# Optimization experiments

Hardware: AMD Instinct MI355X
Metric: run time of the kernel (lower is better)

## Reference

```python
import jax, jax.numpy as jnp
import numpy as np
from jax import lax

B, T, N, HID = 4, 144, 256, 64
CH, NC = 9, 4  # chunk_size_short, num_chunks_short


def setup_inputs():
    key = jax.random.key(0)
    ks = jax.random.split(key, 30)
    r = lambda i, sh, s=0.05: jax.random.normal(ks[i], sh, jnp.float32) * s
    adj = (jax.random.uniform(ks[1], (N, N)) < 0.1).astype(jnp.float32)
    adj = adj.at[jnp.arange(N), jnp.arange(N)].set(1.0)  # self-loops
    return {
        "seg": jax.random.normal(ks[0], (B, T, N, N), jnp.float32),
        "adj": adj,
        "dist": jax.random.uniform(ks[2], (N, N), jnp.float32),
        "W_gat": r(3, (N, HID)),
        "a_src": r(4, (HID,)),
        "a_dst": r(5, (HID,)),
        "lstm_Wih": r(6, (4 * HID, HID)),
        "lstm_Whh": r(7, (4 * HID, HID)),
        "lstm_bih": r(8, (4 * HID,)),
        "lstm_bhh": r(9, (4 * HID,)),
        "attnL_W": r(10, (HID, HID)),
        "attnL_b": r(11, (HID,)),
        "attnL_v": r(12, (HID,)),
        "gru_Wih": r(13, (NC, 3 * HID, HID)),
        "gru_Whh": r(14, (NC, 3 * HID, HID)),
        "gru_bih": r(15, (NC, 3 * HID)),
        "gru_bhh": r(16, (NC, 3 * HID)),
        "attnS_W": r(17, (NC, HID, HID)),
        "attnS_b": r(18, (NC, HID)),
        "attnS_v": r(19, (NC, HID)),
        "lin1_W": r(20, (2 * HID, HID + HID * NC)),
        "lin1_b": r(21, (2 * HID,)),
        "lin2_W": r(22, (N * N, 2 * HID)),
        "lin2_b": r(23, (N * N,)),
        "conv_k": r(24, (1, 1, 3, 3)),
        "conv_b": r(25, (1,)),
    }


def gat_features(seg, adj, dist, W_gat, a_src, a_dst):
    # Batches the per-timestep GAT over the time axis (B,T folded together).
    Wh = jnp.einsum('btnf,fh->btnh', seg, W_gat)                     # (B,T,N,H)
    e = jax.nn.leaky_relu((Wh @ a_src)[..., :, None] + (Wh @ a_dst)[..., None, :], 0.2)
    e = e - dist                                                     # distance penalty on logits
    logits = jnp.where(adj > 0, e, -1e9)                             # mask non-edges
    attn = jax.nn.softmax(logits, axis=-1)                           # (B,T,N,N)
    Hn = jax.nn.elu(jnp.einsum('btij,btjh->btih', attn, Wh))         # (B,T,N,H)
    return Hn.mean(axis=2)                                           # (B,T,H) mean-pool over nodes


def lstm(x, Wih, Whh, bih, bhh):
    h0 = jnp.zeros((x.shape[0], Whh.shape[1]), x.dtype)
    def step(carry, xt):
        h, c = carry
        g = xt @ Wih.T + bih + h @ Whh.T + bhh
        i, f, gg, o = jnp.split(g, 4, axis=-1)  # torch gate order i,f,g,o
        c = jax.nn.sigmoid(f) * c + jax.nn.sigmoid(i) * jnp.tanh(gg)
        h = jax.nn.sigmoid(o) * jnp.tanh(c)
        return (h, c), h
    _, ys = lax.scan(step, (h0, h0), jnp.swapaxes(x, 0, 1))
    return jnp.swapaxes(ys, 0, 1)


def gru(x, Wih, Whh, bih, bhh):
    h0 = jnp.zeros((x.shape[0], Whh.shape[1]), x.dtype)
    def step(h, xt):
        gx = xt @ Wih.T + bih
        gh = h @ Whh.T + bhh
        xr, xz, xn = jnp.split(gx, 3, axis=-1)  # torch gate order r,z,n
        hr, hz, hn = jnp.split(gh, 3, axis=-1)
        rr = jax.nn.sigmoid(xr + hr)
        zz = jax.nn.sigmoid(xz + hz)
        nn_ = jnp.tanh(xn + rr * hn)
        h = (1.0 - zz) * nn_ + zz * h
        return h, h
    _, ys = lax.scan(step, h0, jnp.swapaxes(x, 0, 1))
    return jnp.swapaxes(ys, 0, 1)


def tattn(h, W, b, v):
    s = jnp.tanh(h @ W + b) @ v          # (B,T) additive attention scores
    a = jax.nn.softmax(s, axis=1)
    return jnp.einsum('bt,bth->bh', a, h)


def reference(seg, adj, dist, W_gat, a_src, a_dst, lstm_Wih, lstm_Whh, lstm_bih, lstm_bhh,
              attnL_W, attnL_b, attnL_v, gru_Wih, gru_Whh, gru_bih, gru_bhh,
              attnS_W, attnS_b, attnS_v, lin1_W, lin1_b, lin2_W, lin2_b, conv_k, conv_b):
    Bsz = seg.shape[0]
    feats = gat_features(seg, adj, dist, W_gat, a_src, a_dst)        # (B,T,H)
    ctxL = tattn(lstm(feats, lstm_Wih, lstm_Whh, lstm_bih, lstm_bhh), attnL_W, attnL_b, attnL_v)
    # Short-term GCN features are the same GAT outputs on the last W_short steps.
    short = feats[:, -CH * NC:, :].reshape(Bsz, NC, CH, HID)
    gru_out = jax.vmap(gru, in_axes=(1, 0, 0, 0, 0), out_axes=1)(short, gru_Wih, gru_Whh, gru_bih, gru_bhh)
    ctxS = jax.vmap(tattn, in_axes=(1, 0, 0, 0), out_axes=1)(gru_out, attnS_W, attnS_b, attnS_v)  # (B,NC,H)
    fused = jnp.concatenate([ctxL, ctxS.reshape(Bsz, NC * HID)], axis=1)  # (B, 5H)
    h1 = jax.nn.relu(fused @ lin1_W.T + lin1_b)
    out = (h1 @ lin2_W.T + lin2_b).reshape(Bsz, 1, N, N)
    out = lax.conv_general_dilated(out, conv_k, (1, 1), 'SAME',
                                   dimension_numbers=('NCHW', 'OIHW', 'NCHW'))
    out = out + conv_b[None, :, None, None]
    return jax.nn.softplus(out[:, 0])
```

## Files before the change

kernel.cpp:

```cpp
#include <hip/hip_runtime.h>
#include <hip/hip_bf16.h>
#include <cstddef>


typedef __attribute__((ext_vector_type(8))) short bf16x8;
typedef __attribute__((ext_vector_type(4))) float f32x4;

__device__ __forceinline__ float sigf(float x) { return 1.0f / (1.0f + __expf(-x)); }
__device__ __forceinline__ float tanh_(float x) {
    x = fminf(fmaxf(x, -15.f), 15.f);
    float e = __expf(2.f * x);
    return (e - 1.f) / (e + 1.f);
}
__device__ __forceinline__ unsigned short f2b(float f) {
    unsigned u = __float_as_uint(f);
    u += 0x7FFFu + ((u >> 16) & 1u);
    return (unsigned short)(u >> 16);
}
__device__ __forceinline__ unsigned pk2(float lo, float hi) {
    __hip_bfloat162 h = __float22bfloat162_rn(float2{lo, hi});
    return *reinterpret_cast<unsigned*>(&h);
}
__device__ __forceinline__ float b2f(short s) {
    return __uint_as_float(((unsigned)(unsigned short)s) << 16);
}
__device__ __forceinline__ float rlane(float v, int k) {
    return __uint_as_float(__builtin_amdgcn_readlane(__float_as_uint(v), k));
}

__global__ void k_prep(const float* __restrict__ adj, const float* __restrict__ dist,
                       const float* __restrict__ W_gat,
                       unsigned short* __restrict__ Mb, unsigned short* __restrict__ Wt) {
    int blk = blockIdx.x, tid = threadIdx.x;
    if (blk < 256) {
        int i = blk * 256 + tid;
        Mb[i] = f2b((adj[i] > 0.f) ? -dist[i] : -1e9f);
    } else {
        for (int it = 0; it < 64; ++it) {
            int e = it * 256 + tid;
            int k = e >> 6, c = e & 63;
            Wt[c * 256 + k] = f2b(W_gat[e]);
        }
    }
}

__global__ __launch_bounds__(256, 6) void k_gatA(
    const float* __restrict__ seg, const unsigned short* __restrict__ Wt,
    const float* __restrict__ a_src, const float* __restrict__ a_dst,
    unsigned short* __restrict__ WhT, float* __restrict__ svec, float* __restrict__ dvec,
    float* __restrict__ smaxp, float* __restrict__ dmaxp) {
    __shared__ __align__(16) short A_s[64 * 64];
    __shared__ float red[8];

    const int tid  = threadIdx.x;
    const int lane = tid & 63;
    const int wv   = tid >> 6;
    const int blk  = blockIdx.x;
    const int bt   = blk >> 2;
    const int sub  = blk & 3;
    const float* __restrict__ segp = seg + (size_t)bt * 65536 + sub * 64 * 256;

    f32x4 acc[4];
    #pragma unroll
    for (int n = 0; n < 4; ++n) acc[n] = (f32x4)(0.f);

    for (int kc = 0; kc < 4; ++kc) {
        #pragma unroll
        for (int it = 0; it < 2; ++it) {
            int unit = it * 256 + tid;
            int row = unit >> 3, u = unit & 7;
            const float* g = segp + row * 256 + kc * 64 + u * 8;
            f32x4 v0 = *(const f32x4*)g;
            f32x4 v1 = *(const f32x4*)(g + 4);
            uint4 pk;
            pk.x = pk2(v0[0], v0[1]); pk.y = pk2(v0[2], v0[3]);
            pk.z = pk2(v1[0], v1[1]); pk.w = pk2(v1[2], v1[3]);
            *(uint4*)&A_s[(row * 8 + (u ^ (row & 7))) * 8] = pk;
        }
        bf16x8 bfr[2][4];
        #pragma unroll
        for (int kt2 = 0; kt2 < 2; ++kt2) {
            int ku = kt2 * 4 + (lane >> 4);
            #pragma unroll
            for (int nt = 0; nt < 4; ++nt) {
                int col = nt * 16 + (lane & 15);
                bfr[kt2][nt] = *(const bf16x8*)(Wt + col * 256 + kc * 64 + ku * 8);
            }
        }
        __syncthreads();
        int arow = wv * 16 + (lane & 15);
        #pragma unroll
        for (int kt2 = 0; kt2 < 2; ++kt2) {
            int ku = kt2 * 4 + (lane >> 4);
            bf16x8 afr = *(const bf16x8*)&A_s[(arow * 8 + (ku ^ (arow & 7))) * 8];
            #pragma unroll
            for (int nt = 0; nt < 4; ++nt)
                acc[nt] = __builtin_amdgcn_mfma_f32_16x16x32_bf16(afr, bfr[kt2][nt], acc[nt], 0, 0, 0);
        }
        __syncthreads();
    }

    float asv[4], adv[4];
    #pragma unroll
    for (int nt = 0; nt < 4; ++nt) {
        asv[nt] = a_src[nt * 16 + (lane & 15)];
        adv[nt] = a_dst[nt * 16 + (lane & 15)];
    }
    float mxs = -3e38f, mxd = -3e38f;
    int rowbase = sub * 64 + wv * 16;
    #pragma unroll
    for (int r = 0; r < 4; ++r) {
        float ps = acc[0][r] * asv[0] + acc[1][r] * asv[1] + acc[2][r] * asv[2] + acc[3][r] * asv[3];
        float pd = acc[0][r] * adv[0] + acc[1][r] * adv[1] + acc[2][r] * adv[2] + acc[3][r] * adv[3];
        #pragma unroll
        for (int m = 1; m < 16; m <<= 1) { ps += __shfl_xor(ps, m); pd += __shfl_xor(pd, m); }
        if ((lane & 15) == 0) {
            int row = rowbase + (lane >> 4) * 4 + r;
            svec[bt * 256 + row] = ps;
            dvec[bt * 256 + row] = pd;
        }
        mxs = fmaxf(mxs, ps); mxd = fmaxf(mxd, pd);
    }
    mxs = fmaxf(mxs, __shfl_xor(mxs, 16)); mxs = fmaxf(mxs, __shfl_xor(mxs, 32));
    mxd = fmaxf(mxd, __shfl_xor(mxd, 16)); mxd = fmaxf(mxd, __shfl_xor(mxd, 32));
    if (lane == 0) { red[wv] = mxs; red[4 + wv] = mxd; }

    {
        int c = lane & 15, q = lane >> 4;
        int kt2  = wv >> 1;
        int oct  = (wv & 1) * 2 + (q >> 1);
        int laneP = oct * 16 + c;
        int e0b  = (q & 1) * 8;
        #pragma unroll
        for (int nt = 0; nt < 4; ++nt) {
            uint2 pk4;
            pk4.x = pk2(acc[nt][0], acc[nt][1]);
            pk4.y = pk2(acc[nt][2], acc[nt][3]);
            *(uint2*)((char*)A_s + (((kt2 * 4 + nt) * 64 + laneP) * 16 + e0b)) = pk4;
        }
    }
    __syncthreads();
    {
        const uint4* Fs = (const uint4*)A_s;
        uint4* Gd = (uint4*)(WhT + (size_t)bt * 16384 + sub * 4096);
        Gd[tid] = Fs[tid];
        Gd[256 + tid] = Fs[256 + tid];
    }
    if (tid == 0) {
        smaxp[blk] = fmaxf(fmaxf(red[0], red[1]), fmaxf(red[2], red[3]));
        dmaxp[blk] = fmaxf(fmaxf(red[4], red[5]), fmaxf(red[6], red[7]));
    }
}

__global__ __launch_bounds__(256, 4) void k_gatBF(
    const unsigned short* __restrict__ WhT, const float* __restrict__ svec,
    const float* __restrict__ dvec, const float* __restrict__ smaxp,
    const float* __restrict__ dmaxp, const unsigned short* __restrict__ Mb,
    const float* __restrict__ lWih, const float* __restrict__ lbih,
    const float* __restrict__ lbhh, float* __restrict__ feats, float* __restrict__ gx) {
    __shared__ __align__(16) float dv_l[256];
    __shared__ float red[256];
    __shared__ __align__(16) float feats_l[64];

    const int tid  = threadIdx.x;
    const int lane = tid & 63;
    const int wv   = tid >> 6;
    const int wrow = wv * 64;
    const int bt   = blockIdx.x;
    const unsigned short* __restrict__ Wp = WhT + (size_t)bt * 16384;

    dv_l[tid] = dvec[bt * 256 + tid];
    float mB;
    {
        float ms = fmaxf(fmaxf(smaxp[bt * 4], smaxp[bt * 4 + 1]),
                         fmaxf(smaxp[bt * 4 + 2], smaxp[bt * 4 + 3]));
        float md = fmaxf(fmaxf(dmaxp[bt * 4], dmaxp[bt * 4 + 1]),
                         fmaxf(dmaxp[bt * 4 + 2], dmaxp[bt * 4 + 3]));
        float x = ms + md;
        mB = fmaxf(x, 0.2f * x);
    }
    float sv4[4];
    #pragma unroll
    for (int mt = 0; mt < 4; ++mt) sv4[mt] = svec[bt * 256 + wrow + mt * 16 + (lane & 15)];
    __syncthreads();

    f32x4 acc2[4][4];
    #pragma unroll
    for (int a = 0; a < 4; ++a)
        #pragma unroll
        for (int b = 0; b < 4; ++b) acc2[a][b] = (f32x4)(0.f);
    float psum[4] = {0.f, 0.f, 0.f, 0.f};
    const int jbase = (lane >> 4) * 8;

    #pragma unroll 1
    for (int kt = 0; kt < 8; ++kt) {
        int j0 = kt * 32 + jbase;
        bf16x8 bfr[4];
        #pragma unroll
        for (int nt = 0; nt < 4; ++nt)
            bfr[nt] = *(const bf16x8*)(Wp + ((kt * 4 + nt) * 64 + lane) * 8);
        f32x4 d0 = *(const f32x4*)&dv_l[j0];
        f32x4 d1 = *(const f32x4*)&dv_l[j0 + 4];
        #pragma unroll
        for (int mt = 0; mt < 4; ++mt) {
            int prow = wrow + mt * 16 + (lane & 15);
            bf16x8 mrow = *(const bf16x8*)(Mb + prow * 256 + j0);
            float p[8];
            #pragma unroll
            for (int e = 0; e < 4; ++e) {
                float u = sv4[mt] + d0[e];
                u = fmaxf(u, 0.2f * u);
                p[e] = __expf(u + b2f(mrow[e]) - mB);
                float w = sv4[mt] + d1[e];
                w = fmaxf(w, 0.2f * w);
                p[4 + e] = __expf(w + b2f(mrow[4 + e]) - mB);
            }
            psum[mt] += ((p[0] + p[1]) + (p[2] + p[3])) + ((p[4] + p[5]) + (p[6] + p[7]));
            uint4 upf;
            upf.x = pk2(p[0], p[1]); upf.y = pk2(p[2], p[3]);
            upf.z = pk2(p[4], p[5]); upf.w = pk2(p[6], p[7]);
            bf16x8 pf = *reinterpret_cast<bf16x8*>(&upf);
            #pragma unroll
            for (int nt = 0; nt < 4; ++nt)
                acc2[mt][nt] = __builtin_amdgcn_mfma_f32_16x16x32_bf16(pf, bfr[nt], acc2[mt][nt], 0, 0, 0);
        }
    }
    #pragma unroll
    for (int mt = 0; mt < 4; ++mt) {
        psum[mt] += __shfl_xor(psum[mt], 16);
        psum[mt] += __shfl_xor(psum[mt], 32);
    }

    float part[4] = {0.f, 0.f, 0.f, 0.f};
    #pragma unroll
    for (int mt = 0; mt < 4; ++mt) {
        #pragma unroll
        for (int r = 0; r < 4; ++r) {
            float rs  = __shfl(psum[mt], ((lane >> 4) << 2) + r);
            float inv = 1.0f / rs;
            #pragma unroll
            for (int nt = 0; nt < 4; ++nt) {
                float x = acc2[mt][nt][r] * inv;
                x = (x > 0.f) ? x : expm1f(x);
                part[nt] += x;
            }
        }
    }
    #pragma unroll
    for (int nt = 0; nt < 4; ++nt) {
        part[nt] += __shfl_xor(part[nt], 16);
        part[nt] += __shfl_xor(part[nt], 32);
    }
    if ((lane >> 4) == 0) {
        #pragma unroll
        for (int nt = 0; nt < 4; ++nt) red[wv * 64 + nt * 16 + lane] = part[nt];
    }
    __syncthreads();
    if (tid < 64) {
        float f = (red[tid] + red[64 + tid] + red[128 + tid] + red[192 + tid]) * (1.0f / 256.0f);
        feats[bt * 64 + tid] = f;
        feats_l[tid] = f;
    }
    __syncthreads();
    {
        float a = lbih[tid] + lbhh[tid];
        const float* wp = lWih + tid * 64;
        #pragma unroll
        for (int k4 = 0; k4 < 16; ++k4) {
            f32x4 w = *(const f32x4*)(wp + k4 * 4);
            f32x4 x = *(const f32x4*)&feats_l[k4 * 4];
            a += w[0] * x[0] + w[1] * x[1] + w[2] * x[2] + w[3] * x[3];
        }
        gx[bt * 256 + tid] = a;
    }
}

__global__ __launch_bounds__(256) void k_rnnctx(
    const float* __restrict__ gx, const float* __restrict__ lWhh,
    const float* __restrict__ aLW, const float* __restrict__ aLb, const float* __restrict__ aLv,
    const float* __restrict__ feats, const float* __restrict__ gWih,
    const float* __restrict__ gWhh, const float* __restrict__ gbih,
    const float* __restrict__ gbhh, const float* __restrict__ aSW,
    const float* __restrict__ aSb, const float* __restrict__ aSv,
    float* __restrict__ ctxL, float* __restrict__ ctxS) {
    __shared__ __align__(16) float smem[10048];
    int tid = threadIdx.x;
    if (blockIdx.x < 4) {
        int b = blockIdx.x;
        int lane = tid & 63, wv = tid >> 6;
        float* Hl = smem;
        float* gl = smem + 9216;
        float* sc = smem + 9728;
        float* al = smem + 9872;
        float wr[64];
        #pragma unroll
        for (int q = 0; q < 16; ++q)
            *(f32x4*)&wr[q * 4] = *(const f32x4*)&lWhh[tid * 64 + q * 4];
        float c_s = 0.f;
        float hprev = 0.f;
        float gx_cur = gx[(size_t)b * 36864 + tid];
        for (int t = 0; t < 144; ++t) {
            float gx_next = (t < 143) ? gx[((size_t)b * 144 + t + 1) * 256 + tid] : 0.f;
            float s0 = 0.f, s1 = 0.f, s2 = 0.f, s3 = 0.f;
            #pragma unroll
            for (int k = 0; k < 64; k += 4) {
                s0 += wr[k]     * rlane(hprev, k);
                s1 += wr[k + 1] * rlane(hprev, k + 1);
                s2 += wr[k + 2] * rlane(hprev, k + 2);
                s3 += wr[k + 3] * rlane(hprev, k + 3);
            }
            float a = gx_cur + ((s0 + s1) + (s2 + s3));
            gl[(t & 1) * 256 + tid] = a;
            __syncthreads();
            float ig = gl[(t & 1) * 256 + lane],       fg = gl[(t & 1) * 256 + 64 + lane],
                  gg = gl[(t & 1) * 256 + 128 + lane], og = gl[(t & 1) * 256 + 192 + lane];
            c_s = sigf(fg) * c_s + sigf(ig) * tanh_(gg);
            float h = sigf(og) * tanh_(c_s);
            hprev = h;
            if (wv == 0) Hl[t * 64 + lane] = h;
            gx_cur = gx_next;
        }
        __syncthreads();
        float wcol[64];
        #pragma unroll
        for (int k = 0; k < 64; ++k) wcol[k] = aLW[k * 64 + lane];
        float bb = aLb[lane], vv = aLv[lane];
        for (int g = 0; g < 36; ++g) {
            int t = g * 4 + wv;
            float acc = bb;
            #pragma unroll
            for (int q = 0; q < 16; ++q) {
                f32x4 h4 = *(const f32x4*)&Hl[t * 64 + q * 4];
                acc += wcol[q * 4 + 0] * h4[0] + wcol[q * 4 + 1] * h4[1]
                     + wcol[q * 4 + 2] * h4[2] + wcol[q * 4 + 3] * h4[3];
            }
            float p = tanh_(acc) * vv;
            #pragma unroll
            for (int m = 1; m < 64; m <<= 1) p += __shfl_xor(p, m);
            if (lane == 0) sc[t] = p;
        }
        __syncthreads();
        float mx = -3e38f;
        for (int t2 = 0; t2 < 144; ++t2) mx = fmaxf(mx, sc[t2]);
        float ss = 0.f;
        for (int t2 = 0; t2 < 144; ++t2) ss += __expf(sc[t2] - mx);
        float inv = 1.f / ss;
        if (tid < 144) al[tid] = __expf(sc[tid] - mx) * inv;
        __syncthreads();
        if (tid < 64) {
            float acc = 0.f;
            for (int t2 = 0; t2 < 144; ++t2) acc += al[t2] * Hl[t2 * 64 + tid];
            ctxL[b * 64 + tid] = acc;
        }
    } else {
        int bi_ = blockIdx.x - 4;
        int b = bi_ >> 2, c2 = bi_ & 3;
        float* hvg = smem;
        float* xvg = smem + 64;
        float* gxl = smem + 128;
        float* ghl = smem + 320;
        float* hst = smem + 512;
        float wi[64], wh[64], bi = 0.f, bh = 0.f, h_s = 0.f;
        if (tid < 192) {
            #pragma unroll
            for (int q = 0; q < 16; ++q) {
                *(f32x4*)&wi[q * 4] = *(const f32x4*)&gWih[(size_t)(c2 * 192 + tid) * 64 + q * 4];
                *(f32x4*)&wh[q * 4] = *(const f32x4*)&gWhh[(size_t)(c2 * 192 + tid) * 64 + q * 4];
            }
            bi = gbih[c2 * 192 + tid];
            bh = gbhh[c2 * 192 + tid];
        }
        if (tid < 64) hvg[tid] = 0.f;
        __syncthreads();
        for (int s = 0; s < 9; ++s) {
            int t = 108 + c2 * 9 + s;
            if (tid < 64) xvg[tid] = feats[(b * 144 + t) * 64 + tid];
            __syncthreads();
            if (tid < 192) {
                float ax = bi, ah = bh;
                float a0 = 0.f, a1 = 0.f, b0 = 0.f, b1 = 0.f;
                #pragma unroll
                for (int k = 0; k < 64; k += 2) {
                    a0 += wi[k] * xvg[k];     a1 += wi[k + 1] * xvg[k + 1];
                    b0 += wh[k] * hvg[k];     b1 += wh[k + 1] * hvg[k + 1];
                }
                gxl[tid] = ax + a0 + a1; ghl[tid] = ah + b0 + b1;
            }
            __syncthreads();
            if (tid < 64) {
                float xr = gxl[tid], xz = gxl[64 + tid], xn = gxl[128 + tid];
                float hr = ghl[tid], hz = ghl[64 + tid], hn = ghl[128 + tid];
                float rr = sigf(xr + hr), zz = sigf(xz + hz);
                float nn = tanh_(xn + rr * hn);
                h_s = (1.f - zz) * nn + zz * h_s;
                hvg[tid] = h_s;
                hst[s * 64 + tid] = h_s;
            }
            __syncthreads();
        }
        if (tid < 64) {
            int lane = tid;
            const float* Wc = aSW + c2 * 4096;
            float wcol[64];
            #pragma unroll
            for (int k = 0; k < 64; ++k) wcol[k] = Wc[k * 64 + lane];
            float bb = aSb[c2 * 64 + lane], vv = aSv[c2 * 64 + lane];
            float sv[9];
            #pragma unroll 1
            for (int s = 0; s < 9; ++s) {
                float acc = bb;
                #pragma unroll
                for (int q = 0; q < 16; ++q) {
                    f32x4 h4 = *(const f32x4*)&hst[s * 64 + q * 4];
                    acc += wcol[q * 4 + 0] * h4[0] + wcol[q * 4 + 1] * h4[1]
                         + wcol[q * 4 + 2] * h4[2] + wcol[q * 4 + 3] * h4[3];
                }
                float p = tanh_(acc) * vv;
                #pragma unroll
                for (int m = 1; m < 64; m <<= 1) p += __shfl_xor(p, m);
                sv[s] = p;
            }
            float mx = -3e38f;
            #pragma unroll
            for (int s = 0; s < 9; ++s) mx = fmaxf(mx, sv[s]);
            float ss = 0.f;
            #pragma unroll
            for (int s = 0; s < 9; ++s) { sv[s] = __expf(sv[s] - mx); ss += sv[s]; }
            float inv = 1.f / ss;
            float acc = 0.f;
            #pragma unroll
            for (int s = 0; s < 9; ++s) acc += sv[s] * inv * hst[s * 64 + lane];
            ctxS[(b * 4 + c2) * 64 + lane] = acc;
        }
    }
}

__global__ __launch_bounds__(512) void k_lin1(
    const float* __restrict__ ctxL, const float* __restrict__ ctxS,
    const float* __restrict__ W, const float* __restrict__ bb,
    float* __restrict__ h1) {
    int tid = threadIdx.x;
    __shared__ __align__(16) float fu[4 * 320];
    for (int c = tid; c < 1280; c += 512) {
        int b2 = c / 320, k = c % 320;
        fu[c] = (k < 64) ? ctxL[b2 * 64 + k] : ctxS[b2 * 256 + (k - 64)];
    }
    __syncthreads();
    int b = tid >> 7, r = tid & 127;
    float acc = bb[r];
    #pragma unroll 4
    for (int k4 = 0; k4 < 80; ++k4) {
        f32x4 w = *(const f32x4*)&W[r * 320 + k4 * 4];
        f32x4 x = *(const f32x4*)&fu[b * 320 + k4 * 4];
        acc += w[0] * x[0] + w[1] * x[1] + w[2] * x[2] + w[3] * x[3];
    }
    h1[b * 128 + r] = fmaxf(acc, 0.f);
}

__global__ __launch_bounds__(256) void k_lin2(
    const float* __restrict__ h1, const float* __restrict__ W,
    const float* __restrict__ bb, float* __restrict__ h2) {
    __shared__ __align__(16) float h1l[512];
    int tid = threadIdx.x, blk = blockIdx.x;
    for (int c = tid; c < 512; c += 256) h1l[c] = h1[c];
    __syncthreads();
    int r = blk * 64 + (tid >> 2);
    int q = tid & 3;
    const float* wp = W + (size_t)r * 128 + q * 32;
    float a0 = 0.f, a1 = 0.f, a2 = 0.f, a3 = 0.f;
    #pragma unroll
    for (int i = 0; i < 8; ++i) {
        f32x4 w  = *(const f32x4*)(wp + i * 4);
        f32x4 x0 = *(const f32x4*)&h1l[q * 32 + i * 4];
        f32x4 x1 = *(const f32x4*)&h1l[128 + q * 32 + i * 4];
        f32x4 x2 = *(const f32x4*)&h1l[256 + q * 32 + i * 4];
        f32x4 x3 = *(const f32x4*)&h1l[384 + q * 32 + i * 4];
        a0 += w[0] * x0[0] + w[1] * x0[1] + w[2] * x0[2] + w[3] * x0[3];
        a1 += w[0] * x1[0] + w[1] * x1[1] + w[2] * x1[2] + w[3] * x1[3];
        a2 += w[0] * x2[0] + w[1] * x2[1] + w[2] * x2[2] + w[3] * x2[3];
        a3 += w[0] * x3[0] + w[1] * x3[1] + w[2] * x3[2] + w[3] * x3[3];
    }
    a0 += __shfl_xor(a0, 1); a0 += __shfl_xor(a0, 2);
    a1 += __shfl_xor(a1, 1); a1 += __shfl_xor(a1, 2);
    a2 += __shfl_xor(a2, 1); a2 += __shfl_xor(a2, 2);
    a3 += __shfl_xor(a3, 1); a3 += __shfl_xor(a3, 2);
    if (q == 0) {
        float bv = bb[r];
        h2[r]             = a0 + bv;
        h2[65536 + r]     = a1 + bv;
        h2[2 * 65536 + r] = a2 + bv;
        h2[3 * 65536 + r] = a3 + bv;
    }
}

__global__ __launch_bounds__(256) void k_conv(
    const float* __restrict__ h2, const float* __restrict__ ck,
    const float* __restrict__ cb, float* __restrict__ out) {
    int x = threadIdx.x;
    int b = blockIdx.x >> 8, y = blockIdx.x & 255;
    float kk[9];
    #pragma unroll
    for (int i = 0; i < 9; ++i) kk[i] = ck[i];
    const float* base = h2 + b * 65536;
    float acc = cb[0];
    #pragma unroll
    for (int dy = -1; dy <= 1; ++dy) {
        int yy = y + dy;
        if (yy < 0 || yy > 255) continue;
        #pragma unroll
        for (int dx = -1; dx <= 1; ++dx) {
            int xx = x + dx;
            if (xx < 0 || xx > 255) continue;
            acc += base[yy * 256 + xx] * kk[(dy + 1) * 3 + (dx + 1)];
        }
    }
    float r = (acc > 20.f) ? acc : log1pf(__expf(acc));
    out[b * 65536 + y * 256 + x] = r;
}

extern "C" void kernel_launch(void* const* d_in, const int* in_sizes, int n_in,
                              void* d_out, int out_size, void* d_ws, size_t ws_size,
                              hipStream_t stream) {
    const float* seg   = (const float*)d_in[0];
    const float* adj   = (const float*)d_in[1];
    const float* dist  = (const float*)d_in[2];
    const float* W_gat = (const float*)d_in[3];
    const float* a_src = (const float*)d_in[4];
    const float* a_dst = (const float*)d_in[5];
    const float* lWih  = (const float*)d_in[6];
    const float* lWhh  = (const float*)d_in[7];
    const float* lbih  = (const float*)d_in[8];
    const float* lbhh  = (const float*)d_in[9];
    const float* aLW   = (const float*)d_in[10];
    const float* aLb   = (const float*)d_in[11];
    const float* aLv   = (const float*)d_in[12];
    const float* gWih  = (const float*)d_in[13];
    const float* gWhh  = (const float*)d_in[14];
    const float* gbih  = (const float*)d_in[15];
    const float* gbhh  = (const float*)d_in[16];
    const float* aSW   = (const float*)d_in[17];
    const float* aSb   = (const float*)d_in[18];
    const float* aSv   = (const float*)d_in[19];
    const float* l1W   = (const float*)d_in[20];
    const float* l1b   = (const float*)d_in[21];
    const float* l2W   = (const float*)d_in[22];
    const float* l2b   = (const float*)d_in[23];
    const float* ck    = (const float*)d_in[24];
    const float* cb    = (const float*)d_in[25];
    float* out = (float*)d_out;

    float* ws = (float*)d_ws;
    unsigned short* Mb  = (unsigned short*)ws;
    unsigned short* Wt  = (unsigned short*)(ws + 32768);
    float* svec  = ws + 40960;
    float* dvec  = svec + 147456;
    float* smaxp = dvec + 147456;
    float* dmaxp = smaxp + 2304;
    unsigned short* WhT = (unsigned short*)(dmaxp + 2304);
    float* feats = dmaxp + 2304 + 4718592;
    float* gx    = feats + 36864;
    float* ctxL  = gx + 147456;
    float* ctxS  = ctxL + 256;
    float* h1    = ctxS + 1024;
    float* h2    = h1 + 512;

    k_prep<<<257, 256, 0, stream>>>(adj, dist, W_gat, Mb, Wt);
    k_gatA<<<2304, 256, 0, stream>>>(seg, Wt, a_src, a_dst, WhT, svec, dvec, smaxp, dmaxp);
    k_gatBF<<<576, 256, 0, stream>>>(WhT, svec, dvec, smaxp, dmaxp, Mb, lWih, lbih, lbhh, feats, gx);
    k_rnnctx<<<20, 256, 0, stream>>>(gx, lWhh, aLW, aLb, aLv, feats, gWih, gWhh, gbih, gbhh,
                                     aSW, aSb, aSv, ctxL, ctxS);
    k_lin1<<<1, 512, 0, stream>>>(ctxL, ctxS, l1W, l1b, h1);
    k_lin2<<<1024, 256, 0, stream>>>(h1, l2W, l2b, h2);
    k_conv<<<1024, 256, 0, stream>>>(h2, ck, cb, out);
}
```

Baseline: 236.7 us.

## Run LSTM recurrence in a single wavefront to remove per-step block barriers

The LSTM recurrence now runs in one 64-lane wavefront. Each lane holds all four gate rows of Whh in registers (256 floats), so the per-timestep shared-memory exchange and __syncthreads are gone. The gate inputs are prefetched two steps ahead, and the sigmoid and tanh divides are replaced with hardware reciprocal approximations. The cost is four times more FMAs per lane on the serial path and heavy register pressure, hence launch_bounds(256,1), with a risk of spilling.

```diff
diff --git a/kernel.cpp b/kernel.cpp
--- a/kernel.cpp
+++ b/kernel.cpp
@@ -6,11 +6,12 @@
 typedef __attribute__((ext_vector_type(8))) short bf16x8;
 typedef __attribute__((ext_vector_type(4))) float f32x4;
 
-__device__ __forceinline__ float sigf(float x) { return 1.0f / (1.0f + __expf(-x)); }
+__device__ __forceinline__ float rcp_(float x) { return __builtin_amdgcn_rcpf(x); }
+__device__ __forceinline__ float sigf(float x) { return rcp_(1.0f + __expf(-x)); }
 __device__ __forceinline__ float tanh_(float x) {
     x = fminf(fmaxf(x, -15.f), 15.f);
     float e = __expf(2.f * x);
-    return (e - 1.f) / (e + 1.f);
+    return (e - 1.f) * rcp_(e + 1.f);
 }
 __device__ __forceinline__ unsigned short f2b(float f) {
     unsigned u = __float_as_uint(f);
@@ -275,7 +276,7 @@
     }
 }
 
-__global__ __launch_bounds__(256) void k_rnnctx(
+__global__ __launch_bounds__(256, 1) void k_rnnctx(
     const float* __restrict__ gx, const float* __restrict__ lWhh,
     const float* __restrict__ aLW, const float* __restrict__ aLb, const float* __restrict__ aLv,
     const float* __restrict__ feats, const float* __restrict__ gWih,
@@ -289,36 +290,49 @@
         int b = blockIdx.x;
         int lane = tid & 63, wv = tid >> 6;
         float* Hl = smem;
-        float* gl = smem + 9216;
-        float* sc = smem + 9728;
-        float* al = smem + 9872;
-        float wr[64];
-        #pragma unroll
-        for (int q = 0; q < 16; ++q)
-            *(f32x4*)&wr[q * 4] = *(const f32x4*)&lWhh[tid * 64 + q * 4];
-        float c_s = 0.f;
-        float hprev = 0.f;
-        float gx_cur = gx[(size_t)b * 36864 + tid];
-        for (int t = 0; t < 144; ++t) {
-            float gx_next = (t < 143) ? gx[((size_t)b * 144 + t + 1) * 256 + tid] : 0.f;
-            float s0 = 0.f, s1 = 0.f, s2 = 0.f, s3 = 0.f;
-            #pragma unroll
-            for (int k = 0; k < 64; k += 4) {
-                s0 += wr[k]     * rlane(hprev, k);
-                s1 += wr[k + 1] * rlane(hprev, k + 1);
-                s2 += wr[k + 2] * rlane(hprev, k + 2);
-                s3 += wr[k + 3] * rlane(hprev, k + 3);
-            }
-            float a = gx_cur + ((s0 + s1) + (s2 + s3));
-            gl[(t & 1) * 256 + tid] = a;
-            __syncthreads();
-            float ig = gl[(t & 1) * 256 + lane],       fg = gl[(t & 1) * 256 + 64 + lane],
-                  gg = gl[(t & 1) * 256 + 128 + lane], og = gl[(t & 1) * 256 + 192 + lane];
-            c_s = sigf(fg) * c_s + sigf(ig) * tanh_(gg);
-            float h = sigf(og) * tanh_(c_s);
-            hprev = h;
-            if (wv == 0) Hl[t * 64 + lane] = h;
-            gx_cur = gx_next;
+        float* sc = smem + 9216;
+        float* al = smem + 9360;
+        if (wv == 0) {
+            float wi_[64], wf_[64], wg_[64], wo_[64];
+            #pragma unroll
+            for (int q = 0; q < 16; ++q) {
+                *(f32x4*)&wi_[q * 4] = *(const f32x4*)&lWhh[(size_t)lane * 64 + q * 4];
+                *(f32x4*)&wf_[q * 4] = *(const f32x4*)&lWhh[(size_t)(64 + lane) * 64 + q * 4];
+                *(f32x4*)&wg_[q * 4] = *(const f32x4*)&lWhh[(size_t)(128 + lane) * 64 + q * 4];
+                *(f32x4*)&wo_[q * 4] = *(const f32x4*)&lWhh[(size_t)(192 + lane) * 64 + q * 4];
+            }
+            const float* gxb = gx + (size_t)b * 36864;
+            float c_s = 0.f, h = 0.f;
+            float gA0 = gxb[lane],       gA1 = gxb[64 + lane],
+                  gA2 = gxb[128 + lane], gA3 = gxb[192 + lane];
+            float gB0 = gxb[256 + lane],  gB1 = gxb[320 + lane],
+                  gB2 = gxb[384 + lane],  gB3 = gxb[448 + lane];
+
+            #define LSTM1W_STEP(T, G0, G1, G2, G3)                                   \
+            {                                                                        \
+                int t_ = (T);                                                        \
+                float ai = (G0), af = (G1), ag = (G2), ao = (G3);                    \
+                if (t_ + 2 < 144) {                                                  \
+                    const float* pf_ = gxb + (t_ + 2) * 256;                         \
+                    G0 = pf_[lane];       G1 = pf_[64 + lane];                       \
+                    G2 = pf_[128 + lane]; G3 = pf_[192 + lane];                      \
+                }                                                                    \
+                _Pragma("unroll")                                                    \
+                for (int k = 0; k < 64; ++k) {                                       \
+                    float hk = rlane(h, k);                                          \
+                    ai += wi_[k] * hk; af += wf_[k] * hk;                            \
+                    ag += wg_[k] * hk; ao += wo_[k] * hk;                            \
+                }                                                                    \
+                c_s = sigf(af) * c_s + sigf(ai) * tanh_(ag);                         \
+                h   = sigf(ao) * tanh_(c_s);                                         \
+                Hl[t_ * 64 + lane] = h;                                              \
+            }
+
+            for (int tt = 0; tt < 72; ++tt) {
+                LSTM1W_STEP(2 * tt,     gA0, gA1, gA2, gA3)
+                LSTM1W_STEP(2 * tt + 1, gB0, gB1, gB2, gB3)
+            }
+            #undef LSTM1W_STEP
         }
         __syncthreads();
         float wcol[64];
```

After: 307.4 us. 29.9% more time.
